# Performance work log

Hardware: AMD Instinct MI355X
Metric: run time of the kernel (lower is better)

The kernel has to match this reference:

```python
import jax, jax.numpy as jnp
from jax import lax
import numpy as np

H, W, C = 2160, 3840, 3
CROP = 3  # rows trimmed top and bottom before filtering


def median1d(x, size, axis):
    """Sliding-window median along `axis` with edge padding (matches
    np.pad(mode='edge') + centered window + np.median for odd size)."""
    pad = size // 2
    pw = [(0, 0)] * x.ndim
    pw[axis] = (pad, pad)
    xp = jnp.pad(x, pw, mode='edge')
    n = x.shape[axis]
    # stack the `size` shifted views -> (..., size), median = middle of sort
    windows = jnp.stack(
        [lax.slice_in_dim(xp, i, i + n, axis=axis) for i in range(size)], axis=-1)
    return jnp.sort(windows, axis=-1)[..., size // 2]


def shift1(x, axis):
    """np.pad(x,(1,0),'constant')[:-1] along `axis`: shift forward, zero-fill."""
    pw = [(0, 0)] * x.ndim
    pw[axis] = (1, 0)
    return lax.slice_in_dim(jnp.pad(x, pw), 0, x.shape[axis], axis=axis)


def setup_inputs() -> dict:
    key = jax.random.key(0)
    k1, k2 = jax.random.split(key)
    img = jax.random.normal(k1, (H, W, C), dtype=jnp.float32)
    mask = jax.random.randint(k2, (H, W), 0, 2, dtype=jnp.int32)
    return {"img": img, "mask": mask, "vertical_size": 5}


def reference(img, mask, vertical_size):
    # mask is read but unused by the original module's math.
    x = img[CROP:-CROP]                       # (H-6, W, C)
    # vertical pass: median(v), shift down 1, median(3) along rows
    v = median1d(x, vertical_size, axis=0)
    v = median1d(shift1(v, axis=0), 3, axis=0)
    # horizontal pass (original reuses vertical_size here): along columns
    h = median1d(v, vertical_size, axis=1)
    h = median1d(shift1(h, axis=1), 3, axis=1)
    return h
```

## Files before the change

kernel.cpp:

```cpp
#include <hip/hip_runtime.h>

#define HH    2160
#define WW    3840
#define CROPC 3
#define NN    (HH - 2*CROPC)
#define WFLAT (WW * 3)

constexpr int TY    = 32;
constexpr int TXF   = 192;
constexpr int SX    = TXF + 18;
constexpr int LSTR  = SX + 1;
constexpr int NTH   = 256;
constexpr int TPR   = 8;
constexpr int CHUNK = TXF / TPR;

__device__ __forceinline__ float med3f(float a, float b, float c) {
    return fmaxf(fminf(a, b), fminf(fmaxf(a, b), c));
}
__device__ __forceinline__ float med5f(float a, float b, float c, float d, float e) {
    float t;
    t = fminf(a, b); b = fmaxf(a, b); a = t;
    t = fminf(c, d); d = fmaxf(c, d); c = t;
    t = fminf(a, c); c = fmaxf(a, c); a = t;
    t = fminf(b, d); d = fmaxf(b, d); b = t;
    t = fminf(b, c); c = fmaxf(b, c); b = t;
    return fminf(c, fmaxf(b, e));
}

__global__ __launch_bounds__(NTH) void fused_median(const float* __restrict__ img,
                                                    float* __restrict__ out) {
    __shared__ float v2s[TY * LSTR];

    const int tid = threadIdx.x;
    const int r0 = blockIdx.y * TY;
    const int f0 = blockIdx.x * TXF;

    if (tid < SX) {
        const int ffp = f0 + tid;
        const int c3  = ffp / 3;
        const int ch  = ffp - 3 * c3;
        const int cc  = min(max(c3 - 4, 0), WW - 1);
        const float* colp = img + (size_t)CROPC * WFLAT + (cc * 3 + ch);

        float x0=0.f, x1=0.f, x2=0.f, x3=0.f, x4=0.f, vm2=0.f, vm1=0.f;
        #pragma unroll
        for (int i = 0; i < TY + 6; ++i) {
            const int rr = min(max(r0 - 4 + i, 0), NN - 1);
            const float xn = colp[(size_t)rr * WFLAT];
            x0 = x1; x1 = x2; x2 = x3; x3 = x4; x4 = xn;
            if (i >= 4) {
                const float vc = med5f(x0, x1, x2, x3, x4);
                if (i >= 6) {
                    const int rz = r0 + i - 6;
                    float a = vm2, b = vm1;
                    if (rz == NN - 1) a = b;
                    if (rz == 1)      a = 0.f;
                    if (rz == 0)    { a = 0.f; b = 0.f; }
                    v2s[(i - 6) * LSTR + tid] = med3f(a, b, vc);
                }
                vm2 = vm1; vm1 = vc;
            }
        }
    }
    __syncthreads();

    const int lr    = tid >> 3;
    const int kk    = tid & (TPR - 1);
    const int r_out = r0 + lr;
    if (r_out >= NN) return;

    const float* s = &v2s[lr * LSTR + kk * CHUNK];
    const int cs = f0 / 3 + (CHUNK / 3) * kk;
    const bool edge = (cs <= 1) || (cs + CHUNK / 3 - 1 >= WW - 1);

    float o[CHUNK];
    #pragma unroll
    for (int c = 0; c < 3; ++c) {
        float ss[14];
        #pragma unroll
        for (int j = 0; j < 14; ++j) ss[j] = s[3 * j + c];
        float h[10];
        #pragma unroll
        for (int m = 0; m < 10; ++m)
            h[m] = med5f(ss[m], ss[m+1], ss[m+2], ss[m+3], ss[m+4]);
        if (!edge) {
            #pragma unroll
            for (int n = 0; n < 8; ++n)
                o[3 * n + c] = med3f(h[n], h[n+1], h[n+2]);
        } else {
            #pragma unroll
            for (int n = 0; n < 8; ++n) {
                const int ci = cs + n;
                float A = h[n], B = h[n+1];
                if (ci == WW - 1) A = B;
                if (ci == 1)      A = 0.f;
                if (ci == 0)    { A = 0.f; B = 0.f; }
                o[3 * n + c] = med3f(A, B, h[n+2]);
            }
        }
    }

    float4* op = (float4*)(out + (size_t)r_out * WFLAT + f0 + kk * CHUNK);
    #pragma unroll
    for (int q = 0; q < CHUNK / 4; ++q)
        op[q] = make_float4(o[4*q], o[4*q+1], o[4*q+2], o[4*q+3]);
}

extern "C" void kernel_launch(void* const* d_in, const int* in_sizes, int n_in,
                              void* d_out, int out_size, void* d_ws, size_t ws_size,
                              hipStream_t stream) {
    const float* img = (const float*)d_in[0];
    float* out = (float*)d_out;
    dim3 grid(WFLAT / TXF, (NN + TY - 1) / TY);
    fused_median<<<grid, NTH, 0, stream>>>(img, out);
}
```

Before: 55.93 us.

## Store vertical results in per-channel planar shared memory and issue all row loads upfront

The intermediate vertical-median tile in shared memory moves from interleaved RGB layout to three per-channel planes, so the horizontal pass reads each channel with float4 loads instead of strided scalar reads. The vertical pass also first loads all 38 rows into a register array and then computes the medians, which lets the global loads be issued back to back instead of interleaved with compute. The cost is higher register pressure from the unrolled load array and a slightly larger shared-memory footprint.

```diff
diff --git a/kernel.cpp b/kernel.cpp
--- a/kernel.cpp
+++ b/kernel.cpp
@@ -9,10 +9,13 @@
 constexpr int TY    = 32;
 constexpr int TXF   = 192;
 constexpr int SX    = TXF + 18;
-constexpr int LSTR  = SX + 1;
 constexpr int NTH   = 256;
 constexpr int TPR   = 8;
-constexpr int CHUNK = TXF / TPR;
+constexpr int XROWS = TY + 6;
+
+constexpr int PC    = SX / 3 + 0;
+constexpr int PSTR  = 76;
+constexpr int PLANE = TY * PSTR + 8;
 
 __device__ __forceinline__ float med3f(float a, float b, float c) {
     return fmaxf(fminf(a, b), fminf(fmaxf(a, b), c));
@@ -29,37 +32,38 @@
 
 __global__ __launch_bounds__(NTH) void fused_median(const float* __restrict__ img,
                                                     float* __restrict__ out) {
-    __shared__ float v2s[TY * LSTR];
+    __shared__ float v2s[3 * PLANE];
 
     const int tid = threadIdx.x;
     const int r0 = blockIdx.y * TY;
     const int f0 = blockIdx.x * TXF;
 
     if (tid < SX) {
-        const int ffp = f0 + tid;
-        const int c3  = ffp / 3;
-        const int ch  = ffp - 3 * c3;
-        const int cc  = min(max(c3 - 4, 0), WW - 1);
+        const int ch   = tid % 3;
+        const int pcol = tid / 3;
+        const int cc   = min(max(f0 / 3 - 4 + pcol, 0), WW - 1);
         const float* colp = img + (size_t)CROPC * WFLAT + (cc * 3 + ch);
 
-        float x0=0.f, x1=0.f, x2=0.f, x3=0.f, x4=0.f, vm2=0.f, vm1=0.f;
+        float xv[XROWS];
         #pragma unroll
-        for (int i = 0; i < TY + 6; ++i) {
+        for (int i = 0; i < XROWS; ++i) {
             const int rr = min(max(r0 - 4 + i, 0), NN - 1);
-            const float xn = colp[(size_t)rr * WFLAT];
-            x0 = x1; x1 = x2; x2 = x3; x3 = x4; x4 = xn;
-            if (i >= 4) {
-                const float vc = med5f(x0, x1, x2, x3, x4);
-                if (i >= 6) {
-                    const int rz = r0 + i - 6;
-                    float a = vm2, b = vm1;
-                    if (rz == NN - 1) a = b;
-                    if (rz == 1)      a = 0.f;
-                    if (rz == 0)    { a = 0.f; b = 0.f; }
-                    v2s[(i - 6) * LSTR + tid] = med3f(a, b, vc);
-                }
-                vm2 = vm1; vm1 = vc;
+            xv[i] = colp[(size_t)rr * WFLAT];
+        }
+
+        float vm2 = 0.f, vm1 = 0.f;
+        #pragma unroll
+        for (int i = 4; i < XROWS; ++i) {
+            const float vc = med5f(xv[i-4], xv[i-3], xv[i-2], xv[i-1], xv[i]);
+            if (i >= 6) {
+                const int rz = r0 + i - 6;
+                float a = vm2, b = vm1;
+                if (rz == NN - 1) a = b;
+                if (rz == 1)      a = 0.f;
+                if (rz == 0)    { a = 0.f; b = 0.f; }
+                v2s[ch * PLANE + (i - 6) * PSTR + pcol] = med3f(a, b, vc);
             }
+            vm2 = vm1; vm1 = vc;
         }
     }
     __syncthreads();
@@ -69,16 +73,19 @@
     const int r_out = r0 + lr;
     if (r_out >= NN) return;
 
-    const float* s = &v2s[lr * LSTR + kk * CHUNK];
-    const int cs = f0 / 3 + (CHUNK / 3) * kk;
-    const bool edge = (cs <= 1) || (cs + CHUNK / 3 - 1 >= WW - 1);
+    const int cbase = f0 / 3 + 8 * kk;
+    const bool edge = (cbase <= 1) || (cbase + 7 >= WW - 1);
 
-    float o[CHUNK];
+    float o[24];
     #pragma unroll
     for (int c = 0; c < 3; ++c) {
-        float ss[14];
-        #pragma unroll
-        for (int j = 0; j < 14; ++j) ss[j] = s[3 * j + c];
+        const float* pb = &v2s[c * PLANE + lr * PSTR + 8 * kk];
+        const float4 q0 = *(const float4*)(pb);
+        const float4 q1 = *(const float4*)(pb + 4);
+        const float4 q2 = *(const float4*)(pb + 8);
+        const float4 q3 = *(const float4*)(pb + 12);
+        const float ss[16] = {q0.x,q0.y,q0.z,q0.w, q1.x,q1.y,q1.z,q1.w,
+                              q2.x,q2.y,q2.z,q2.w, q3.x,q3.y,q3.z,q3.w};
         float h[10];
         #pragma unroll
         for (int m = 0; m < 10; ++m)
@@ -86,23 +93,23 @@
         if (!edge) {
             #pragma unroll
             for (int n = 0; n < 8; ++n)
-                o[3 * n + c] = med3f(h[n], h[n+1], h[n+2]);
+                o[3*n + c] = med3f(h[n], h[n+1], h[n+2]);
         } else {
             #pragma unroll
             for (int n = 0; n < 8; ++n) {
-                const int ci = cs + n;
+                const int ci = cbase + n;
                 float A = h[n], B = h[n+1];
                 if (ci == WW - 1) A = B;
                 if (ci == 1)      A = 0.f;
                 if (ci == 0)    { A = 0.f; B = 0.f; }
-                o[3 * n + c] = med3f(A, B, h[n+2]);
+                o[3*n + c] = med3f(A, B, h[n+2]);
             }
         }
     }
 
-    float4* op = (float4*)(out + (size_t)r_out * WFLAT + f0 + kk * CHUNK);
+    float4* op = (float4*)(out + (size_t)r_out * WFLAT + f0 + 24 * kk);
     #pragma unroll
-    for (int q = 0; q < CHUNK / 4; ++q)
+    for (int q = 0; q < 6; ++q)
         op[q] = make_float4(o[4*q], o[4*q+1], o[4*q+2], o[4*q+3]);
 }
 
```

Result: faster. 51.83 us (-7.3%).
